# Optimization experiments

Measured on AMD Instinct MI355X. Metric: run time of the kernel, lower is better.

The kernel has to match this reference:

```python
import jax, jax.numpy as jnp
import numpy as np

DIM = 64
MAX_DISP = 10
HEAD_SIZE = 8
HEAD_NUM = DIM // HEAD_SIZE
FREQ = 200.0
EPS = 1e-5


def _inv_freq(dim):
    ch = int(np.ceil(dim / 4) * 2)  # 32 for dim=64
    return jnp.asarray(1.0 / FREQ ** (np.arange(0, ch, 2, dtype=np.float32) / ch)), ch


def _interleave_sincos(sin_inp):
    # stack sin/cos on a new last axis then flatten -> [s0,c0,s1,c1,...]
    emb = jnp.stack([jnp.sin(sin_inp), jnp.cos(sin_inp)], axis=-1)
    return emb.reshape(sin_inp.shape[:-1] + (sin_inp.shape[-1] * 2,))


def layernorm2d(x, w, b):
    mean = x.mean(axis=(1, 2, 3), keepdims=True)
    std = jnp.std(x, axis=(1, 2, 3), ddof=1, keepdims=True)  # torch std is unbiased
    x = (x - mean) / (std + EPS)
    return w[None, :, None, None] * x + b[None, :, None, None]


def pos_enc_2d(batch, dim, H, W):
    inv_freq, ch = _inv_freq(dim)
    pos_x = jnp.arange(-(H // 2), H - H // 2, dtype=jnp.float32)
    pos_y = jnp.arange(-(W // 2), W - W // 2, dtype=jnp.float32)
    emb_x = _interleave_sincos(pos_x[:, None] * inv_freq[None, :])  # (H, ch)
    emb_y = _interleave_sincos(pos_y[:, None] * inv_freq[None, :])  # (W, ch)
    emb = jnp.zeros((dim, H, W), dtype=jnp.float32)
    emb = emb.at[0::2].set(jnp.broadcast_to(emb_x.T[:, :, None], (ch, H, W)))
    emb = emb.at[1::2].set(jnp.broadcast_to(emb_y.T[:, None, :], (ch, H, W)))
    return jnp.broadcast_to(emb[None], (batch, dim, H, W))


def pos_enc_2d_rec(homo, dim, H, W):
    B = homo.shape[0]
    inv_freq, ch = _inv_freq(dim)
    l = inv_freq.shape[0]
    pos_x = jnp.arange(-(H // 2), H - H // 2, dtype=jnp.float32)
    pos_y = jnp.arange(-(W // 2), W - W // 2, dtype=jnp.float32)
    X, Y = jnp.meshgrid(pos_x, pos_y, indexing='ij')
    pts = jnp.stack([X.reshape(-1), Y.reshape(-1), jnp.ones(H * W, jnp.float32)], axis=0)  # (3, HW)
    rot = jnp.einsum('bij,jn->bin', homo, pts)  # (B, 3, HW)
    sin_x = rot[:, 0, :, None] * inv_freq[None, None, :]  # (B, HW, l)
    sin_y = rot[:, 1, :, None] * inv_freq[None, None, :]
    emb_x = _interleave_sincos(sin_x).reshape(B, H, W, 2 * l).transpose(0, 3, 1, 2)
    emb_y = _interleave_sincos(sin_y).reshape(B, H, W, 2 * l).transpose(0, 3, 1, 2)
    emb = jnp.zeros((B, dim, H, W), dtype=jnp.float32)
    emb = emb.at[:, 0::2].set(emb_x)
    emb = emb.at[:, 1::2].set(emb_y)
    return emb


def setup_inputs() -> dict:
    key = jax.random.key(0)
    k1, k2, k3, k4, k5 = jax.random.split(key, 5)
    B, H, W = 4, 192, 640
    return {
        'left_image': jax.random.normal(k1, (B, DIM, H, W), jnp.float32),
        'right_image': jax.random.normal(k2, (B, DIM, H, W), jnp.float32),
        'homo': jax.random.normal(k3, (B, 3, 3), jnp.float32),
        'ln_w': jnp.ones((DIM,), jnp.float32),
        'ln_b': jnp.zeros((DIM,), jnp.float32),
        'gp_w': jax.random.normal(k4, (MAX_DISP, HEAD_NUM), jnp.float32) * 0.1,
        'gp_b': jax.random.normal(k5, (MAX_DISP,), jnp.float32) * 0.1,
    }


def reference(left_image, right_image, homo, ln_w, ln_b, gp_w, gp_b):
    B, C, H, W = left_image.shape
    left = layernorm2d(left_image, ln_w, ln_b) + pos_enc_2d(B, C, H, W)
    right = layernorm2d(right_image, ln_w, ln_b) + pos_enc_2d_rec(homo, C, H, W)
    left_h = left.reshape(B, HEAD_NUM, HEAD_SIZE, H, W)
    costs = []
    for d in range(MAX_DISP):  # small fixed loop over disparities
        rs = jnp.roll(right, d + 1, axis=3).reshape(B, HEAD_NUM, HEAD_SIZE, H, W)
        costs.append(jnp.sum(left_h * rs, axis=2))  # (B, HEAD_NUM, H, W)
    cv = jnp.stack(costs, axis=1)  # (B, D, HEAD_NUM, H, W)
    # grouped 1x1 conv: group d maps HEAD_NUM channels -> 1 channel
    out_cv = jnp.einsum('bdghw,dg->bdhw', cv, gp_w) + gp_b[None, :, None, None]
    return jnp.concatenate([left_image, out_cv], axis=1)
```

## Files before the change

### kernel.cpp

```cpp
#include <hip/hip_runtime.h>
#include <cmath>

#define C_ 64
#define H_ 192
#define W_ 640
#define BATCH 4
#define OUTC 74
#define DISP 10
#define WT 64

constexpr long SLICE = (long)C_ * H_ * W_;
constexpr int RED_BLOCKS = 512;
constexpr long N4 = SLICE / 4;

__global__ __launch_bounds__(256)
void stats_kernel(const float* __restrict__ left, const float* __restrict__ right,
                  double* __restrict__ acc)
{
    int bid = blockIdx.x;
    int slice = bid / RED_BLOCKS;
    int blk = bid - slice * RED_BLOCKS;
    const float* src = ((slice < BATCH) ? left : right) + (long)(slice & 3) * SLICE;
    const float4* src4 = (const float4*)src;

    double s = 0.0, s2 = 0.0;
    for (long i = (long)blk * 256 + threadIdx.x; i < N4; i += (long)RED_BLOCKS * 256) {
        float4 v = src4[i];
        s  += ((double)v.x + (double)v.y) + ((double)v.z + (double)v.w);
        s2 += ((double)v.x * v.x + (double)v.y * v.y)
            + ((double)v.z * v.z + (double)v.w * v.w);
    }
#pragma unroll
    for (int off = 32; off; off >>= 1) {
        s  += __shfl_down(s, off);
        s2 += __shfl_down(s2, off);
    }
    __shared__ double sh[8];
    int lane = threadIdx.x & 63, wid = threadIdx.x >> 6;
    if (lane == 0) { sh[wid] = s; sh[4 + wid] = s2; }
    __syncthreads();
    if (threadIdx.x == 0) {
        double ts  = sh[0] + sh[1] + sh[2] + sh[3];
        double ts2 = sh[4] + sh[5] + sh[6] + sh[7];
        atomicAdd(&acc[slice * 2], ts);
        atomicAdd(&acc[slice * 2 + 1], ts2);
    }
}

__global__ void finalize_kernel(const double* __restrict__ acc, float* __restrict__ stats)
{
    int t = threadIdx.x;
    if (t < 8) {
        double S = acc[t * 2], S2 = acc[t * 2 + 1];
        double N = (double)SLICE;
        double mean = S / N;
        double var = (S2 - S * S / N) / (N - 1.0);
        if (var < 0.0) var = 0.0;
        double sd = sqrt(var);
        stats[t]     = (float)mean;
        stats[8 + t] = (float)(1.0 / (sd + 1e-5));
    }
}

__global__ __launch_bounds__(256)
void main_kernel(const float* __restrict__ left, const float* __restrict__ right,
                 const float* __restrict__ homo, const float* __restrict__ lnw,
                 const float* __restrict__ lnb, const float* __restrict__ gpw,
                 const float* __restrict__ gpb, const float* __restrict__ stats,
                 float* __restrict__ out)
{
    int bid = blockIdx.x;
    int wblk = bid % (W_ / WT);
    int h = (bid / (W_ / WT)) % H_;
    int b = bid / ((W_ / WT) * H_);
    int w0 = wblk * WT;
    int tid = threadIdx.x;

    __shared__ float l_s[C_][WT + 1];
    __shared__ float r_s[C_][WT + 10 + 1];
    __shared__ float freq_s[16];
    __shared__ float gpw_s[80];
    __shared__ float lnw_s[C_], lnb_s[C_];

    if (tid < 16) freq_s[tid] = exp2f(-(float)tid * 0.47774101186092114f);
    if (tid < 80) gpw_s[tid] = gpw[tid];
    if (tid < C_) { lnw_s[tid] = lnw[tid]; lnb_s[tid] = lnb[tid]; }

    float h00 = homo[b * 9 + 0], h01 = homo[b * 9 + 1], h02 = homo[b * 9 + 2];
    float h10 = homo[b * 9 + 3], h11 = homo[b * 9 + 4], h12 = homo[b * 9 + 5];
    float mean_l = stats[b],     rstd_l = stats[8 + b];
    float mean_r = stats[4 + b], rstd_r = stats[12 + b];
    float px = (float)(h - H_ / 2);

    __syncthreads();

    long in_base  = ((long)b * C_   * H_ + h) * W_;
    long out_base = ((long)b * OUTC * H_ + h) * W_;

    for (int idx = tid; idx < C_ * WT; idx += 256) {
        int c = idx >> 6, w = idx & 63;
        int gw = w0 + w;
        float raw = left[in_base + (long)c * H_ * W_ + gw];
        out[out_base + (long)c * H_ * W_ + gw] = raw;
        float v = (raw - mean_l) * rstd_l * lnw_s[c] + lnb_s[c];
        int k = c >> 1, j = k >> 1;
        float base = (c & 1) ? (float)(gw - W_ / 2) : px;
        float arg = base * freq_s[j];
        float pe = (k & 1) ? cosf(arg) : sinf(arg);
        l_s[c][w] = v + pe;
    }

    for (int idx = tid; idx < C_ * (WT + 10); idx += 256) {
        int c = idx / (WT + 10), wsi = idx - c * (WT + 10);
        int gw = w0 - 10 + wsi;
        if (gw < 0) gw += W_;
        float raw = right[in_base + (long)c * H_ * W_ + gw];
        float v = (raw - mean_r) * rstd_r * lnw_s[c] + lnb_s[c];
        float py = (float)(gw - W_ / 2);
        float rot = (c & 1) ? (h10 * px + h11 * py + h12)
                            : (h00 * px + h01 * py + h02);
        int k = c >> 1, j = k >> 1;
        float arg = rot * freq_s[j];
        float pe = (k & 1) ? cosf(arg) : sinf(arg);
        r_s[c][wsi] = v + pe;
    }
    __syncthreads();

    int pix = tid >> 2, q = tid & 3;
    float wgt[2][10];
#pragma unroll
    for (int d = 0; d < DISP; ++d) {
        wgt[0][d] = gpw_s[d * 8 + 2 * q];
        wgt[1][d] = gpw_s[d * 8 + 2 * q + 1];
    }
    float acc[10] = {0, 0, 0, 0, 0, 0, 0, 0, 0, 0};
    int c0 = q * 16;
#pragma unroll
    for (int i = 0; i < 16; ++i) {
        int c = c0 + i;
        float lv = l_s[c][pix];
        const float* rrow = &r_s[c][pix];
#pragma unroll
        for (int d = 0; d < DISP; ++d)
            acc[d] = fmaf(lv * rrow[9 - d], wgt[i >> 3][d], acc[d]);
    }
#pragma unroll
    for (int d = 0; d < DISP; ++d) {
        acc[d] += __shfl_xor(acc[d], 1);
        acc[d] += __shfl_xor(acc[d], 2);
    }
#pragma unroll
    for (int m = 0; m < 3; ++m) {
        int d = q + 4 * m;
        if (d < DISP)
            out[out_base + (long)(C_ + d) * H_ * W_ + w0 + pix] = acc[d] + gpb[d];
    }
}

extern "C" void kernel_launch(void* const* d_in, const int* in_sizes, int n_in,
                              void* d_out, int out_size, void* d_ws, size_t ws_size,
                              hipStream_t stream)
{
    const float* left  = (const float*)d_in[0];
    const float* right = (const float*)d_in[1];
    const float* homo  = (const float*)d_in[2];
    const float* lnw   = (const float*)d_in[3];
    const float* lnb   = (const float*)d_in[4];
    const float* gpw   = (const float*)d_in[5];
    const float* gpb   = (const float*)d_in[6];
    float* out = (float*)d_out;

    double* acc  = (double*)d_ws;
    float* stats = (float*)((char*)d_ws + 128);

    hipMemsetAsync(d_ws, 0, 128, stream);
    stats_kernel<<<RED_BLOCKS * 8, 256, 0, stream>>>(left, right, acc);
    finalize_kernel<<<1, 64, 0, stream>>>(acc, stats);
    main_kernel<<<BATCH * H_ * (W_ / WT), 256, 0, stream>>>(
        left, right, homo, lnw, lnb, gpw, gpb, stats, out);
}
```

Baseline: 524.4 us.

## Vectorize input staging with float4, use fast sin/cos, float stats accumulation

The main kernel's left/right staging loops now load and store float4 vectors, fold layernorm into a single FMA, and compute the positional-encoding phase once per channel for row-constant channels. The right halo is loaded separately with float4 reads. Accurate sinf/cosf are replaced by range-reduced __sinf/__cosf, and the stats kernel accumulates per-thread sums in float before converting to double for the reduction. These cut instruction count and transcendental cost, at the price of lower precision in the positional encoding and in the variance sums.

```diff
diff --git a/kernel.cpp b/kernel.cpp
--- a/kernel.cpp
+++ b/kernel.cpp
@@ -8,10 +8,22 @@
 #define OUTC 74
 #define DISP 10
 #define WT 64
+#define HW_ (H_ * W_)
 
 constexpr long SLICE = (long)C_ * H_ * W_;
 constexpr int RED_BLOCKS = 512;
 constexpr long N4 = SLICE / 4;
+
+__device__ __forceinline__ float fsin(float x) {
+    float k = rintf(x * 0.15915494309189535f);
+    float xr = fmaf(k, -6.283185307179586f, x);
+    return __sinf(xr);
+}
+__device__ __forceinline__ float fcos(float x) {
+    float k = rintf(x * 0.15915494309189535f);
+    float xr = fmaf(k, -6.283185307179586f, x);
+    return __cosf(xr);
+}
 
 __global__ __launch_bounds__(256)
 void stats_kernel(const float* __restrict__ left, const float* __restrict__ right,
@@ -23,21 +35,21 @@
     const float* src = ((slice < BATCH) ? left : right) + (long)(slice & 3) * SLICE;
     const float4* src4 = (const float4*)src;
 
-    double s = 0.0, s2 = 0.0;
+    float s = 0.f, s2 = 0.f;
     for (long i = (long)blk * 256 + threadIdx.x; i < N4; i += (long)RED_BLOCKS * 256) {
         float4 v = src4[i];
-        s  += ((double)v.x + (double)v.y) + ((double)v.z + (double)v.w);
-        s2 += ((double)v.x * v.x + (double)v.y * v.y)
-            + ((double)v.z * v.z + (double)v.w * v.w);
-    }
+        s  += (v.x + v.y) + (v.z + v.w);
+        s2 += fmaf(v.x, v.x, v.y * v.y) + fmaf(v.z, v.z, v.w * v.w);
+    }
+    double ds = (double)s, ds2 = (double)s2;
 #pragma unroll
     for (int off = 32; off; off >>= 1) {
-        s  += __shfl_down(s, off);
-        s2 += __shfl_down(s2, off);
+        ds  += __shfl_down(ds, off);
+        ds2 += __shfl_down(ds2, off);
     }
     __shared__ double sh[8];
     int lane = threadIdx.x & 63, wid = threadIdx.x >> 6;
-    if (lane == 0) { sh[wid] = s; sh[4 + wid] = s2; }
+    if (lane == 0) { sh[wid] = ds; sh[4 + wid] = ds2; }
     __syncthreads();
     if (threadIdx.x == 0) {
         double ts  = sh[0] + sh[1] + sh[2] + sh[3];
@@ -91,38 +103,90 @@
     float mean_l = stats[b],     rstd_l = stats[8 + b];
     float mean_r = stats[4 + b], rstd_r = stats[12 + b];
     float px = (float)(h - H_ / 2);
+    float rb0 = fmaf(h00, px, h02);
+    float rb1 = fmaf(h10, px, h12);
 
     __syncthreads();
 
     long in_base  = ((long)b * C_   * H_ + h) * W_;
     long out_base = ((long)b * OUTC * H_ + h) * W_;
 
-    for (int idx = tid; idx < C_ * WT; idx += 256) {
-        int c = idx >> 6, w = idx & 63;
-        int gw = w0 + w;
-        float raw = left[in_base + (long)c * H_ * W_ + gw];
-        out[out_base + (long)c * H_ * W_ + gw] = raw;
-        float v = (raw - mean_l) * rstd_l * lnw_s[c] + lnb_s[c];
-        int k = c >> 1, j = k >> 1;
-        float base = (c & 1) ? (float)(gw - W_ / 2) : px;
-        float arg = base * freq_s[j];
-        float pe = (k & 1) ? cosf(arg) : sinf(arg);
-        l_s[c][w] = v + pe;
-    }
-
-    for (int idx = tid; idx < C_ * (WT + 10); idx += 256) {
-        int c = idx / (WT + 10), wsi = idx - c * (WT + 10);
-        int gw = w0 - 10 + wsi;
-        if (gw < 0) gw += W_;
-        float raw = right[in_base + (long)c * H_ * W_ + gw];
-        float v = (raw - mean_r) * rstd_r * lnw_s[c] + lnb_s[c];
-        float py = (float)(gw - W_ / 2);
-        float rot = (c & 1) ? (h10 * px + h11 * py + h12)
-                            : (h00 * px + h01 * py + h02);
-        int k = c >> 1, j = k >> 1;
-        float arg = rot * freq_s[j];
-        float pe = (k & 1) ? cosf(arg) : sinf(arg);
-        r_s[c][wsi] = v + pe;
+    for (int idx = tid; idx < C_ * 16; idx += 256) {
+        int c = idx >> 4;
+        int w4 = (idx & 15) << 2;
+        int gw = w0 + w4;
+        float4 rv = *(const float4*)(left + in_base + (long)c * HW_ + gw);
+        *(float4*)(out + out_base + (long)c * HW_ + gw) = rv;
+        float r[4] = {rv.x, rv.y, rv.z, rv.w};
+        float g = rstd_l * lnw_s[c];
+        float bb = fmaf(-mean_l, g, lnb_s[c]);
+        int kk = c >> 1, j = kk >> 1;
+        float fr = freq_s[j];
+        bool cc = kk & 1;
+        if (c & 1) {
+#pragma unroll
+            for (int jj = 0; jj < 4; ++jj) {
+                float arg = (float)(gw + jj - W_ / 2) * fr;
+                float pe = cc ? fcos(arg) : fsin(arg);
+                l_s[c][w4 + jj] = fmaf(r[jj], g, bb) + pe;
+            }
+        } else {
+            float arg = px * fr;
+            float pe = cc ? fcos(arg) : fsin(arg);
+#pragma unroll
+            for (int jj = 0; jj < 4; ++jj)
+                l_s[c][w4 + jj] = fmaf(r[jj], g, bb) + pe;
+        }
+    }
+
+    for (int idx = tid; idx < C_ * 16; idx += 256) {
+        int c = idx >> 4;
+        int w4 = (idx & 15) << 2;
+        int gw = w0 + w4;
+        float4 rv = *(const float4*)(right + in_base + (long)c * HW_ + gw);
+        float r[4] = {rv.x, rv.y, rv.z, rv.w};
+        float g = rstd_r * lnw_s[c];
+        float bb = fmaf(-mean_r, g, lnb_s[c]);
+        int kk = c >> 1, j = kk >> 1;
+        float fr = freq_s[j];
+        bool cc = kk & 1;
+        bool odd = c & 1;
+        float rb = odd ? rb1 : rb0;
+        float hy = odd ? h11 : h01;
+#pragma unroll
+        for (int jj = 0; jj < 4; ++jj) {
+            float py = (float)(gw + jj - W_ / 2);
+            float arg = fmaf(hy, py, rb) * fr;
+            float pe = cc ? fcos(arg) : fsin(arg);
+            r_s[c][10 + w4 + jj] = fmaf(r[jj], g, bb) + pe;
+        }
+    }
+
+    for (int idx = tid; idx < C_ * 3; idx += 256) {
+        int c = (idx * 683) >> 11;
+        int t = idx - c * 3;
+        int gw4 = w0 - 12 + 4 * t;
+        if (gw4 < 0) gw4 += W_;
+        float4 rv = *(const float4*)(right + in_base + (long)c * HW_ + gw4);
+        float r[4] = {rv.x, rv.y, rv.z, rv.w};
+        float g = rstd_r * lnw_s[c];
+        float bb = fmaf(-mean_r, g, lnb_s[c]);
+        int kk = c >> 1, j = kk >> 1;
+        float fr = freq_s[j];
+        bool cc = kk & 1;
+        bool odd = c & 1;
+        float rb = odd ? rb1 : rb0;
+        float hy = odd ? h11 : h01;
+#pragma unroll
+        for (int jj = 0; jj < 4; ++jj) {
+            int wsi = 4 * t + jj - 2;
+            if ((unsigned)wsi < 10u) {
+                float py = (float)(gw4 + jj - W_ / 2);
+                float arg = fmaf(hy, py, rb) * fr;
+                float pe = cc ? fcos(arg) : fsin(arg);
+                r_s[c][wsi] = fmaf(r[jj], g, bb) + pe;
+            }
+        }
     }
     __syncthreads();
 
@@ -153,7 +217,7 @@
     for (int m = 0; m < 3; ++m) {
         int d = q + 4 * m;
         if (d < DISP)
-            out[out_base + (long)(C_ + d) * H_ * W_ + w0 + pix] = acc[d] + gpb[d];
+            out[out_base + (long)(C_ + d) * HW_ + w0 + pix] = acc[d] + gpb[d];
     }
 }
 
```

After: 452.7 us. 1.16x faster.
